# Optimization experiments

Hardware: AMD Instinct MI355X
Metric: run time of the kernel (lower is better)

The kernel has to match this reference:

```python
import jax, jax.numpy as jnp
import numpy as np

C, H, V, N, T = 256, 256, 10000, 8, 256


def _residual_mlp(x, w1, b1, w2, b2, w3, b3):
    # ResidualLayerOld: relu(lin2(relu(lin1(x)))) + x, then final Linear
    h = jax.nn.relu(x @ w1 + b1)
    h = jax.nn.relu(h @ w2 + b2) + x
    return h @ w3 + b3


def setup_inputs() -> dict:
    key = jax.random.key(0)
    ks = jax.random.split(key, 16)
    p = lambda k, shape: jax.random.normal(k, shape, jnp.float32) * 0.02
    return dict(
        text=jax.random.randint(ks[0], (N, T), 0, V),
        mask=jnp.ones((N, T), dtype=bool),
        lengths=jnp.full((N,), T - 1, dtype=jnp.int32),  # full-length sequences
        start_emb=jax.random.normal(ks[1], (C, H), jnp.float32),
        state_emb=jax.random.normal(ks[2], (C, H), jnp.float32),
        preterminal_emb=jax.random.normal(ks[3], (C, H), jnp.float32),
        start_w1=p(ks[4], (H, H)), start_b1=jnp.zeros((H,), jnp.float32),
        start_w2=p(ks[5], (H, H)), start_b2=jnp.zeros((H,), jnp.float32),
        start_w3=p(ks[6], (H, 1)), start_b3=jnp.zeros((1,), jnp.float32),
        trans_w1=p(ks[7], (H, H)), trans_b1=jnp.zeros((H,), jnp.float32),
        trans_w2=p(ks[8], (H, H)), trans_b2=jnp.zeros((H,), jnp.float32),
        trans_w3=p(ks[9], (H, C)), trans_b3=jnp.zeros((C,), jnp.float32),
        term_w1=p(ks[10], (H, H)), term_b1=jnp.zeros((H,), jnp.float32),
        term_w2=p(ks[11], (H, H)), term_b2=jnp.zeros((H,), jnp.float32),
        term_w3=p(ks[12], (H, V)), term_b3=jnp.zeros((V,), jnp.float32),
    )


def _score(text, mask, lengths,
           start_emb, state_emb, preterminal_emb,
           start_w1, start_b1, start_w2, start_b2, start_w3, start_b3,
           trans_w1, trans_b1, trans_w2, trans_b2, trans_w3, trans_b3,
           term_w1, term_b1, term_w2, term_b2, term_w3, term_b3):
    n, t = text.shape
    c = state_emb.shape[0]
    # start / transition / emission distributions (dropout_type == 'none')
    init = jax.nn.log_softmax(
        _residual_mlp(start_emb, start_w1, start_b1, start_w2, start_b2, start_w3, start_b3)[:, 0], -1)  # [C]
    trans = jax.nn.log_softmax(
        _residual_mlp(state_emb, trans_w1, trans_b1, trans_w2, trans_b2, trans_w3, trans_b3), -1)  # [C,C]
    log_em = jax.nn.log_softmax(
        _residual_mlp(preterminal_emb, term_w1, term_b1, term_w2, term_b2, term_w3, term_b3), -1)  # [C,V]
    obs = log_em.T[text]  # [N,T,C], log p(x_t | z=c)
    # torch_struct LinearChain.hmm edge potentials: phi[n,t,c_next,c_prev]
    phi = trans[None, None] + obs[:, 1:, :, None]  # [N,T-1,C,C]
    phi = phi.at[:, 0].add(init[None, None, :] + obs[:, 0][:, None, :])
    phi_t = jnp.swapaxes(phi, 0, 1)  # [T-1,N,C,C]

    def fwd_step(alpha, p):
        new = jax.nn.logsumexp(p + alpha[:, None, :], axis=-1)  # reduce over c_prev
        return new, new

    _, alphas = jax.lax.scan(fwd_step, jnp.zeros((n, c), phi.dtype), phi_t)  # [T-1,N,C]

    def bwd_step(beta, p):
        new = jax.nn.logsumexp(p + beta[:, :, None], axis=1)  # reduce over c_next
        return new, beta

    _, betas = jax.lax.scan(bwd_step, jnp.zeros((n, c), phi.dtype), phi_t, reverse=True)  # [T-1,N,C]

    alpha_prev = jnp.concatenate([jnp.zeros((1, n, c), phi.dtype), alphas[:-1]], 0)
    log_Z = jax.nn.logsumexp(alphas[-1], -1)  # [N]
    # edge posteriors
    log_m = alpha_prev[:, :, None, :] + phi_t + betas[:, :, :, None] - log_Z[None, :, None, None]
    marginals = jnp.swapaxes(jnp.exp(log_m), 0, 1)  # [N,T-1,C,C]

    evidence = jax.nn.logsumexp(alphas[lengths - 1, jnp.arange(n)], -1).sum()
    elbo = jnp.where(mask[:, 1:, None, None],
                     jax.lax.stop_gradient(marginals) * phi,
                     0.0).sum()
    return elbo, evidence


def reference(text, mask, lengths,
              start_emb, state_emb, preterminal_emb,
              start_w1, start_b1, start_w2, start_b2, start_w3, start_b3,
              trans_w1, trans_b1, trans_w2, trans_b2, trans_w3, trans_b3,
              term_w1, term_b1, term_w2, term_b2, term_w3, term_b3):
    elbo, evidence = _score(text, mask, lengths,
                            start_emb, state_emb, preterminal_emb,
                            start_w1, start_b1, start_w2, start_b2, start_w3, start_b3,
                            trans_w1, trans_b1, trans_w2, trans_b2, trans_w3, trans_b3,
                            term_w1, term_b1, term_w2, term_b2, term_w3, term_b3)
    return elbo, evidence
```

## Files before the change

kernel.cpp:

```cpp
#include <hip/hip_runtime.h>
#include <hip/hip_bf16.h>

#define C_ 256
#define H_ 256
#define V_ 10000
#define N_ 8
#define T_ 256
#define TM1_ 255
#define NB_ ((V_ + 31) / 32)
#define VT_ ((V_ + 31) / 32)
#define CH_ 32
#define NCH_ (T_ / CH_)

typedef _Float16 h2_t __attribute__((ext_vector_type(2)));
typedef _Float16 h4_t __attribute__((ext_vector_type(4)));
typedef _Float16 h8_t __attribute__((ext_vector_type(8)));
typedef float f4v __attribute__((ext_vector_type(4)));

__device__ __forceinline__ void bar_lgkm() {
  asm volatile("s_waitcnt lgkmcnt(0)\ns_barrier" ::: "memory");
}

__device__ __forceinline__ float wave_red_max(float v) {
#define DPP_MAX(ctrl) { int iv_ = __float_as_int(v); \
  int r_ = __builtin_amdgcn_update_dpp(iv_, iv_, ctrl, 0xF, 0xF, false); \
  v = fmaxf(v, __int_as_float(r_)); }
  DPP_MAX(0x111) DPP_MAX(0x112) DPP_MAX(0x114) DPP_MAX(0x118)
  DPP_MAX(0x142) DPP_MAX(0x143)
#undef DPP_MAX
  return __int_as_float(__builtin_amdgcn_readlane(__float_as_int(v), 63));
}
__device__ __forceinline__ float wave_red_sum(float v) {
#define DPP_ADD(ctrl) { \
  int r_ = __builtin_amdgcn_update_dpp(0, __float_as_int(v), ctrl, 0xF, 0xF, true); \
  v += __int_as_float(r_); }
  DPP_ADD(0x111) DPP_ADD(0x112) DPP_ADD(0x114) DPP_ADD(0x118)
  DPP_ADD(0x142) DPP_ADD(0x143)
#undef DPP_ADD
  return __int_as_float(__builtin_amdgcn_readlane(__float_as_int(v), 63));
}

__device__ __forceinline__ float block_allmax(float v, float* red) {
  v = wave_red_max(v);
  if ((threadIdx.x & 63) == 0) red[threadIdx.x >> 6] = v;
  __syncthreads();
  v = fmaxf(fmaxf(red[0], red[1]), fmaxf(red[2], red[3]));
  __syncthreads();
  return v;
}
__device__ __forceinline__ float block_allsum(float v, float* red) {
  v = wave_red_sum(v);
  if ((threadIdx.x & 63) == 0) red[threadIdx.x >> 6] = v;
  __syncthreads();
  v = (red[0] + red[1]) + (red[2] + red[3]);
  __syncthreads();
  return v;
}

__global__ __launch_bounds__(256) void k_w3t(const float* __restrict__ w3,
                                             float* __restrict__ w3T) {
  __shared__ float t_s[32][33];
  const int tx = threadIdx.x & 31;
  const int ty = threadIdx.x >> 5;
  const int v0 = blockIdx.x * 32;
  const int k0 = blockIdx.y * 32;
#pragma unroll
  for (int r = 0; r < 4; ++r) {
    int k = k0 + ty + r * 8;
    int v = v0 + tx;
    if (v < V_) t_s[ty + r * 8][tx] = w3[k * V_ + v];
  }
  __syncthreads();
#pragma unroll
  for (int r = 0; r < 4; ++r) {
    int v = v0 + ty + r * 8;
    if (v < V_) w3T[(size_t)v * H_ + k0 + tx] = t_s[tx][ty + r * 8];
  }
}

__device__ __forceinline__ void mlp4(
    const float* __restrict__ emb,
    const float* __restrict__ w1, const float* __restrict__ b1,
    const float* __restrict__ w2, const float* __restrict__ b2,
    int r0, float (&e_s)[4][C_], float (&h_s)[4][C_], float (&h2_s)[4][C_]) {
  const int tid = threadIdx.x;
#pragma unroll
  for (int rr = 0; rr < 4; ++rr)
    e_s[rr][tid] = emb[(r0 + rr) * H_ + tid];
  __syncthreads();
  float bb = b1[tid];
  float a0 = bb, a1 = bb, a2 = bb, a3 = bb;
  for (int k4 = 0; k4 < H_ / 4; ++k4) {
    float4 e0 = ((const float4*)e_s[0])[k4];
    float4 e1 = ((const float4*)e_s[1])[k4];
    float4 e2 = ((const float4*)e_s[2])[k4];
    float4 e3 = ((const float4*)e_s[3])[k4];
    const float* wp = w1 + (k4 * 4) * H_ + tid;
    float wa = wp[0], wb = wp[H_], wc = wp[2 * H_], wd = wp[3 * H_];
    a0 = fmaf(e0.x, wa, a0); a0 = fmaf(e0.y, wb, a0);
    a0 = fmaf(e0.z, wc, a0); a0 = fmaf(e0.w, wd, a0);
    a1 = fmaf(e1.x, wa, a1); a1 = fmaf(e1.y, wb, a1);
    a1 = fmaf(e1.z, wc, a1); a1 = fmaf(e1.w, wd, a1);
    a2 = fmaf(e2.x, wa, a2); a2 = fmaf(e2.y, wb, a2);
    a2 = fmaf(e2.z, wc, a2); a2 = fmaf(e2.w, wd, a2);
    a3 = fmaf(e3.x, wa, a3); a3 = fmaf(e3.y, wb, a3);
    a3 = fmaf(e3.z, wc, a3); a3 = fmaf(e3.w, wd, a3);
  }
  h_s[0][tid] = fmaxf(a0, 0.f);
  h_s[1][tid] = fmaxf(a1, 0.f);
  h_s[2][tid] = fmaxf(a2, 0.f);
  h_s[3][tid] = fmaxf(a3, 0.f);
  __syncthreads();
  bb = b2[tid];
  a0 = bb; a1 = bb; a2 = bb; a3 = bb;
  for (int k4 = 0; k4 < H_ / 4; ++k4) {
    float4 e0 = ((const float4*)h_s[0])[k4];
    float4 e1 = ((const float4*)h_s[1])[k4];
    float4 e2 = ((const float4*)h_s[2])[k4];
    float4 e3 = ((const float4*)h_s[3])[k4];
    const float* wp = w2 + (k4 * 4) * H_ + tid;
    float wa = wp[0], wb = wp[H_], wc = wp[2 * H_], wd = wp[3 * H_];
    a0 = fmaf(e0.x, wa, a0); a0 = fmaf(e0.y, wb, a0);
    a0 = fmaf(e0.z, wc, a0); a0 = fmaf(e0.w, wd, a0);
    a1 = fmaf(e1.x, wa, a1); a1 = fmaf(e1.y, wb, a1);
    a1 = fmaf(e1.z, wc, a1); a1 = fmaf(e1.w, wd, a1);
    a2 = fmaf(e2.x, wa, a2); a2 = fmaf(e2.y, wb, a2);
    a2 = fmaf(e2.z, wc, a2); a2 = fmaf(e2.w, wd, a2);
    a3 = fmaf(e3.x, wa, a3); a3 = fmaf(e3.y, wb, a3);
    a3 = fmaf(e3.z, wc, a3); a3 = fmaf(e3.w, wd, a3);
  }
  h2_s[0][tid] = fmaxf(a0, 0.f) + e_s[0][tid];
  h2_s[1][tid] = fmaxf(a1, 0.f) + e_s[1][tid];
  h2_s[2][tid] = fmaxf(a2, 0.f) + e_s[2][tid];
  h2_s[3][tid] = fmaxf(a3, 0.f) + e_s[3][tid];
  __syncthreads();
}

__global__ __launch_bounds__(256) void k_start(
    const float* __restrict__ emb, const float* __restrict__ w1,
    const float* __restrict__ b1, const float* __restrict__ w2,
    const float* __restrict__ b2, const float* __restrict__ w3,
    const float* __restrict__ b3, float* __restrict__ slogit) {
  __shared__ __align__(16) float e_s[4][C_], h_s[4][C_], h2_s[4][C_];
  __shared__ float red[4];
  const int r0 = blockIdx.x * 4;
  const int tid = threadIdx.x;
  mlp4(emb, w1, b1, w2, b2, r0, e_s, h_s, h2_s);
  float w3v = w3[tid];
  float s0 = block_allsum(h2_s[0][tid] * w3v, red);
  float s1 = block_allsum(h2_s[1][tid] * w3v, red);
  float s2 = block_allsum(h2_s[2][tid] * w3v, red);
  float s3 = block_allsum(h2_s[3][tid] * w3v, red);
  if (tid == 0) {
    float bb = b3[0];
    slogit[r0 + 0] = s0 + bb;
    slogit[r0 + 1] = s1 + bb;
    slogit[r0 + 2] = s2 + bb;
    slogit[r0 + 3] = s3 + bb;
  }
}

__global__ void k_init(const float* __restrict__ slogit, float* __restrict__ initv) {
  __shared__ float red[4];
  const int tid = threadIdx.x;
  float x = slogit[tid];
  float m = block_allmax(x, red);
  float se = block_allsum(__expf(x - m), red);
  initv[tid] = x - m - __logf(se);
}

__global__ __launch_bounds__(256) void k_trans(
    const float* __restrict__ emb, const float* __restrict__ w1,
    const float* __restrict__ b1, const float* __restrict__ w2,
    const float* __restrict__ b2, const float* __restrict__ w3,
    const float* __restrict__ b3, float* __restrict__ Pf,
    float* __restrict__ PLf, float* __restrict__ PTf,
    _Float16* __restrict__ P_h, _Float16* __restrict__ PT_h) {
  __shared__ __align__(16) float e_s[4][C_], h_s[4][C_], h2_s[4][C_];
  __shared__ float red[4];
  const int r0 = blockIdx.x * 4;
  const int tid = threadIdx.x;
  mlp4(emb, w1, b1, w2, b2, r0, e_s, h_s, h2_s);
  float lb = b3[tid];
  float l0 = lb, l1 = lb, l2 = lb, l3 = lb;
  for (int k4 = 0; k4 < H_ / 4; ++k4) {
    float4 e0 = ((const float4*)h2_s[0])[k4];
    float4 e1 = ((const float4*)h2_s[1])[k4];
    float4 e2 = ((const float4*)h2_s[2])[k4];
    float4 e3 = ((const float4*)h2_s[3])[k4];
    const float* wp = w3 + (k4 * 4) * C_ + tid;
    float wa = wp[0], wb = wp[C_], wc = wp[2 * C_], wd = wp[3 * C_];
    l0 = fmaf(e0.x, wa, l0); l0 = fmaf(e0.y, wb, l0);
    l0 = fmaf(e0.z, wc, l0); l0 = fmaf(e0.w, wd, l0);
    l1 = fmaf(e1.x, wa, l1); l1 = fmaf(e1.y, wb, l1);
    l1 = fmaf(e1.z, wc, l1); l1 = fmaf(e1.w, wd, l1);
    l2 = fmaf(e2.x, wa, l2); l2 = fmaf(e2.y, wb, l2);
    l2 = fmaf(e2.z, wc, l2); l2 = fmaf(e2.w, wd, l2);
    l3 = fmaf(e3.x, wa, l3); l3 = fmaf(e3.y, wb, l3);
    l3 = fmaf(e3.z, wc, l3); l3 = fmaf(e3.w, wd, l3);
  }
  float lg[4] = {l0, l1, l2, l3};
#pragma unroll
  for (int rr = 0; rr < 4; ++rr) {
    float m = block_allmax(lg[rr], red);
    float e = __expf(lg[rr] - m);
    float se = block_allsum(e, red);
    float p = e / se;
    float tv = lg[rr] - m - __logf(se);
    const int r = r0 + rr;
    Pf[r * C_ + tid] = p;
    PLf[r * C_ + tid] = p * tv;
    PTf[tid * C_ + r] = p;
    P_h[r * C_ + tid] = (_Float16)p;
    PT_h[tid * C_ + r] = (_Float16)p;
  }
}

__global__ __launch_bounds__(256) void k_term_mlp(
    const float* __restrict__ emb, const float* __restrict__ w1,
    const float* __restrict__ b1, const float* __restrict__ w2,
    const float* __restrict__ b2, float* __restrict__ H2,
    float* __restrict__ H2T) {
  __shared__ __align__(16) float e_s[4][C_], h_s[4][C_], h2_s[4][C_];
  const int r0 = blockIdx.x * 4;
  const int tid = threadIdx.x;
  mlp4(emb, w1, b1, w2, b2, r0, e_s, h_s, h2_s);
#pragma unroll
  for (int rr = 0; rr < 4; ++rr) {
    const int r = r0 + rr;
    float v = h2_s[rr][tid];
    H2[r * H_ + tid] = v;
    H2T[tid * C_ + r] = v;
  }
}

__global__ __launch_bounds__(256) void k_term_stats(
    const float* __restrict__ H2, const float* __restrict__ w3,
    const float* __restrict__ b3, float* __restrict__ partm,
    float* __restrict__ parts) {
  __shared__ __align__(16) float w3_s[H_][32];
  __shared__ float b3_s[32];
  const int v0 = blockIdx.x * 32;
  const int tid = threadIdx.x;
  const int ncols = min(32, V_ - v0);
  for (int idx = tid; idx < H_ * 32; idx += 256) {
    int k = idx >> 5, c = idx & 31;
    w3_s[k][c] = (c < ncols) ? w3[k * V_ + v0 + c] : 0.f;
  }
  if (tid < 32) b3_s[tid] = (tid < ncols) ? b3[v0 + tid] : 0.f;
  __syncthreads();
  float acc[32];
#pragma unroll
  for (int c = 0; c < 32; ++c) acc[c] = 0.f;
  const float4* hq = (const float4*)(H2 + tid * H_);
  for (int k4 = 0; k4 < H_ / 4; ++k4) {
    float4 h = hq[k4];
    float hk[4];
    *(float4*)hk = h;
#pragma unroll
    for (int kk = 0; kk < 4; ++kk) {
      float hv = hk[kk];
      const int k = k4 * 4 + kk;
      const float4* wq = (const float4*)(&w3_s[k][0]);
#pragma unroll
      for (int c4 = 0; c4 < 8; ++c4) {
        float4 w = wq[c4];
        acc[c4 * 4 + 0] = fmaf(hv, w.x, acc[c4 * 4 + 0]);
        acc[c4 * 4 + 1] = fmaf(hv, w.y, acc[c4 * 4 + 1]);
        acc[c4 * 4 + 2] = fmaf(hv, w.z, acc[c4 * 4 + 2]);
        acc[c4 * 4 + 3] = fmaf(hv, w.w, acc[c4 * 4 + 3]);
      }
    }
  }
  float m = -1e30f;
#pragma unroll
  for (int c = 0; c < 32; ++c) {
    acc[c] += b3_s[c];
    if (c < ncols) m = fmaxf(m, acc[c]);
  }
  float se = 0.f;
#pragma unroll
  for (int c = 0; c < 32; ++c)
    if (c < ncols) se += __expf(acc[c] - m);
  partm[blockIdx.x * C_ + tid] = m;
  parts[blockIdx.x * C_ + tid] = se;
}

__global__ void k_denom(const float* __restrict__ partm,
                        const float* __restrict__ parts,
                        float* __restrict__ denom) {
  const int r = threadIdx.x;
  float m = -1e30f;
#pragma unroll 8
  for (int b = 0; b < NB_; ++b) m = fmaxf(m, partm[b * C_ + r]);
  float s = 0.f;
#pragma unroll 8
  for (int b = 0; b < NB_; ++b)
    s += parts[b * C_ + r] * __expf(partm[b * C_ + r] - m);
  denom[r] = m + __logf(s);
}

__global__ __launch_bounds__(256) void k_obs4(
    const int* __restrict__ text, const float* __restrict__ H2T,
    const float* __restrict__ w3T, const float* __restrict__ b3,
    const float* __restrict__ denom, float* __restrict__ EOBS,
    _Float16* __restrict__ EOBSh, float* __restrict__ Karr) {
  __shared__ __align__(16) float w_s[H_][8];
  __shared__ float redm[4][8];
  const int c = threadIdx.x;
  const int wid = c >> 6;
  const int lane = c & 63;
  const int base = blockIdx.x * 8;
  int tok[8];
#pragma unroll
  for (int i = 0; i < 8; ++i) tok[i] = text[base + i];
  float wtmp[8];
#pragma unroll
  for (int i = 0; i < 8; ++i) wtmp[i] = w3T[(size_t)tok[i] * H_ + c];
  float b3t[8];
#pragma unroll
  for (int i = 0; i < 8; ++i) b3t[i] = b3[tok[i]];
#pragma unroll
  for (int i = 0; i < 8; ++i) w_s[c][i] = wtmp[i];
  __syncthreads();
  float acc[8];
#pragma unroll
  for (int i = 0; i < 8; ++i) acc[i] = 0.f;
  for (int k4 = 0; k4 < H_ / 4; ++k4) {
    float hv[4];
#pragma unroll
    for (int kk = 0; kk < 4; ++kk) hv[kk] = H2T[(k4 * 4 + kk) * C_ + c];
#pragma unroll
    for (int kk = 0; kk < 4; ++kk) {
      const float4* wq = (const float4*)(&w_s[k4 * 4 + kk][0]);
      float4 wa = wq[0], wb = wq[1];
      acc[0] = fmaf(hv[kk], wa.x, acc[0]);
      acc[1] = fmaf(hv[kk], wa.y, acc[1]);
      acc[2] = fmaf(hv[kk], wa.z, acc[2]);
      acc[3] = fmaf(hv[kk], wa.w, acc[3]);
      acc[4] = fmaf(hv[kk], wb.x, acc[4]);
      acc[5] = fmaf(hv[kk], wb.y, acc[5]);
      acc[6] = fmaf(hv[kk], wb.z, acc[6]);
      acc[7] = fmaf(hv[kk], wb.w, acc[7]);
    }
  }
  float dn = denom[c];
  float obsv[8];
#pragma unroll
  for (int i = 0; i < 8; ++i) obsv[i] = acc[i] + b3t[i] - dn;
#pragma unroll
  for (int i = 0; i < 8; ++i) {
    float wm = wave_red_max(obsv[i]);
    if (lane == 0) redm[wid][i] = wm;
  }
  __syncthreads();
#pragma unroll
  for (int i = 0; i < 8; ++i) {
    float Ki = fmaxf(fmaxf(redm[0][i], redm[1][i]),
                     fmaxf(redm[2][i], redm[3][i]));
    float ev = __expf(obsv[i] - Ki);
    EOBS[(base + i) * C_ + c] = ev;
    EOBSh[(size_t)(base + i) * C_ + c] = (_Float16)ev;
    if (c == 0) Karr[base + i] = Ki;
  }
}

__global__ __launch_bounds__(256, 1) void k_scan6(
    const _Float16* __restrict__ P_h, const _Float16* __restrict__ PT_h,
    const float* __restrict__ initv, const float* __restrict__ EOBS,
    const _Float16* __restrict__ EOBSh, const float* __restrict__ Karr,
    float* __restrict__ AL, float* __restrict__ BL, float* __restrict__ CC,
    float* __restrict__ DD, float* __restrict__ LOGZ) {
  __shared__ __align__(16) _Float16 eobuf[2][CH_][C_];
  __shared__ __align__(16) _Float16 ubuf[2][C_];
  __shared__ float Kbuf[T_];
  __shared__ float red[4];
  const int tid = threadIdx.x;
  const int wave = tid >> 6;
  const int lane = tid & 63;
  const int quad = lane >> 4;
  const int nn16 = lane & 15;
  const bool bwd = blockIdx.x >= N_;
  const int n = blockIdx.x & (N_ - 1);
  const _Float16* __restrict__ M = bwd ? PT_h : P_h;
  const _Float16* __restrict__ eb = EOBSh + (size_t)n * T_ * C_;

  h8_t afrag[4][8];
#pragma unroll
  for (int mt = 0; mt < 4; ++mt) {
    const _Float16* rp = M + (size_t)((wave << 6) + (mt << 4) + nn16) * C_ + (quad << 3);
#pragma unroll
    for (int kt = 0; kt < 8; ++kt)
      afrag[mt][kt] = *(const h8_t*)(rp + (kt << 5));
  }
  const int stb = (wave << 6) + (quad << 2);

  Kbuf[tid] = Karr[n * T_ + tid];
  {
    const int c0 = bwd ? (NCH_ - 1) : 0;
    const h8_t* g = (const h8_t*)(eb + (size_t)c0 * CH_ * C_);
    h8_t v0 = g[tid], v1 = g[256 + tid], v2 = g[512 + tid], v3 = g[768 + tid];
    h8_t* d = (h8_t*)&eobuf[c0 & 1][0][0];
    d[tid] = v0; d[256 + tid] = v1; d[512 + tid] = v2; d[768 + tid] = v3;
  }
  h8_t pend0, pend1, pend2, pend3;
  {
    const int c1 = bwd ? (NCH_ - 2) : 1;
    const h8_t* g = (const h8_t*)(eb + (size_t)c1 * CH_ * C_);
    pend0 = g[tid]; pend1 = g[256 + tid]; pend2 = g[512 + tid]; pend3 = g[768 + tid];
  }
  __syncthreads();

  if (!bwd) {
    float K0 = Karr[n * T_];
    f4v x0[4];
    float lmax = -1e30f;
#pragma unroll
    for (int mt = 0; mt < 4; ++mt) {
      const int st0 = stb + (mt << 4);
      f4v iv = *(const f4v*)(initv + st0);
      f4v e0 = *(const f4v*)(EOBS + (size_t)(n * T_) * C_ + st0);
#pragma unroll
      for (int r = 0; r < 4; ++r) {
        x0[mt][r] = iv[r] + __logf(e0[r]) + K0;
        lmax = fmaxf(lmax, x0[mt][r]);
      }
    }
    float wm = wave_red_max(lmax);
    if (lane == 0) red[wave] = wm;
    __syncthreads();
    float m0 = fmaxf(fmaxf(red[0], red[1]), fmaxf(red[2], red[3]));
    __syncthreads();
    float Cacc = m0;
    f4v uval[4];
#pragma unroll
    for (int mt = 0; mt < 4; ++mt) {
      const int st0 = stb + (mt << 4);
#pragma unroll
      for (int r = 0; r < 4; ++r) uval[mt][r] = __expf(x0[mt][r] - m0);
      if (nn16 == 0) {
        h4_t p;
#pragma unroll
        for (int r = 0; r < 4; ++r) p[r] = (_Float16)uval[mt][r];
        *(h4_t*)(&ubuf[0][st0]) = p;
        *(f4v*)(AL + (size_t)(0 * N_ + n) * C_ + st0) = uval[mt];
      }
    }
    if (tid == 0) CC[0 * N_ + n] = Cacc;
    float invm = 1.f, logm = 0.f;
    __syncthreads();

#pragma unroll 1
    for (int t = 0; t < TM1_; ++t) {
      const int e = t + 1;
      const int slot = e & 31;
      const int par = (e >> 5) & 1;
      const int cur = t & 1, nxt = cur ^ 1;
      const bool resc = (t & 3) == 3;
      h8_t bf[8];
#pragma unroll
      for (int kt = 0; kt < 8; ++kt)
        bf[kt] = *(const h8_t*)(&ubuf[cur][(kt << 5) + (quad << 3)]);
      h4_t eoh[4];
#pragma unroll
      for (int mt = 0; mt < 4; ++mt)
        eoh[mt] = *(const h4_t*)(&eobuf[par][slot][stb + (mt << 4)]);
      float KA = Kbuf[e];
      f4v ae[4], ao[4];
#pragma unroll
      for (int mt = 0; mt < 4; ++mt) { ae[mt] = (f4v){0, 0, 0, 0}; ao[mt] = (f4v){0, 0, 0, 0}; }
#pragma unroll
      for (int kt = 0; kt < 8; kt += 2) {
#pragma unroll
        for (int mt = 0; mt < 4; ++mt)
          ae[mt] = __builtin_amdgcn_mfma_f32_16x16x32_f16(afrag[mt][kt], bf[kt], ae[mt], 0, 0, 0);
#pragma unroll
        for (int mt = 0; mt < 4; ++mt)
          ao[mt] = __builtin_amdgcn_mfma_f32_16x16x32_f16(afrag[mt][kt + 1], bf[kt + 1], ao[mt], 0, 0, 0);
      }
#pragma unroll
      for (int mt = 0; mt < 4; ++mt) {
#pragma unroll
        for (int r = 0; r < 4; ++r)
          uval[mt][r] = (ae[mt][r] + ao[mt][r]) * invm * (float)eoh[mt][r];
      }
      Cacc += KA + logm;
      if (nn16 == 0) {
#pragma unroll
        for (int mt = 0; mt < 4; ++mt) {
          const int st0 = stb + (mt << 4);
          h4_t p;
#pragma unroll
          for (int r = 0; r < 4; ++r) p[r] = (_Float16)uval[mt][r];
          *(h4_t*)(&ubuf[nxt][st0]) = p;
        }
      }
      if (resc) {
        float lmx = -1e30f;
#pragma unroll
        for (int mt = 0; mt < 4; ++mt)
#pragma unroll
          for (int r = 0; r < 4; ++r) lmx = fmaxf(lmx, uval[mt][r]);
        float wmm = wave_red_max(lmx);
        if (lane == 0) red[wave] = wmm;
      }
      if (slot == 31 && e != 255) {
        const int ci = e >> 5;
        h8_t* d = (h8_t*)&eobuf[(ci + 1) & 1][0][0];
        d[tid] = pend0; d[256 + tid] = pend1; d[512 + tid] = pend2; d[768 + tid] = pend3;
        if (ci + 2 < NCH_) {
          const h8_t* g = (const h8_t*)(eb + (size_t)(ci + 2) * CH_ * C_);
          pend0 = g[tid]; pend1 = g[256 + tid]; pend2 = g[512 + tid]; pend3 = g[768 + tid];
        }
      }
      bar_lgkm();
      if (nn16 == 0) {
#pragma unroll
        for (int mt = 0; mt < 4; ++mt)
          *(f4v*)(AL + (size_t)((t + 1) * N_ + n) * C_ + stb + (mt << 4)) = uval[mt];
      }
      if (tid == 0) CC[(t + 1) * N_ + n] = Cacc;
      if (resc) {
        float m = fmaxf(fmaxf(red[0], red[1]), fmaxf(red[2], red[3]));
        m = fmaxf(m, 1e-30f);
        invm = 1.f / m;
        logm = __logf(m);
      } else { invm = 1.f; logm = 0.f; }
    }
    float s = 0.f;
#pragma unroll
    for (int mt = 0; mt < 4; ++mt)
      s += (uval[mt][0] + uval[mt][1]) + (uval[mt][2] + uval[mt][3]);
    s = wave_red_sum(s);
    if (lane == 0) red[wave] = s;
    __syncthreads();
    float S = ((red[0] + red[1]) + (red[2] + red[3])) * (1.f / 16.f);
    if (tid == 0) LOGZ[n] = __logf(S) + Cacc;
  } else {
    float Dacc = 0.f;
    f4v vval[4];
#pragma unroll
    for (int mt = 0; mt < 4; ++mt) {
      const int st0 = stb + (mt << 4);
      vval[mt] = *(const f4v*)(EOBS + ((size_t)n * T_ + TM1_) * C_ + st0);
      if (nn16 == 0) {
        h4_t p;
#pragma unroll
        for (int r = 0; r < 4; ++r) p[r] = (_Float16)vval[mt][r];
        *(h4_t*)(&ubuf[0][st0]) = p;
        f4v one = (f4v){1.f, 1.f, 1.f, 1.f};
        *(f4v*)(BL + (size_t)((TM1_ - 1) * N_ + n) * C_ + st0) = one;
      }
    }
    if (tid == 0) DD[(TM1_ - 1) * N_ + n] = 0.f;
    __syncthreads();

#pragma unroll 1
    for (int it = 0, t = TM1_ - 2; t >= 0; --t, ++it) {
      const int e = t + 1;
      const int slot = e & 31;
      const int par = (e >> 5) & 1;
      const int cur = it & 1, nxt = cur ^ 1;
      float invm = 1.f, logm = 0.f;
      if ((it & 3) == 3) {
        float m = fmaxf(fmaxf(red[0], red[1]), fmaxf(red[2], red[3]));
        m = fmaxf(m, 1e-30f);
        invm = 1.f / m;
        logm = __logf(m);
      }
      h8_t bf[8];
#pragma unroll
      for (int kt = 0; kt < 8; ++kt)
        bf[kt] = *(const h8_t*)(&ubuf[cur][(kt << 5) + (quad << 3)]);
      h4_t eoh[4];
#pragma unroll
      for (int mt = 0; mt < 4; ++mt)
        eoh[mt] = *(const h4_t*)(&eobuf[par][slot][stb + (mt << 4)]);
      float KA = Kbuf[e + 1];
      f4v ae[4], ao[4];
#pragma unroll
      for (int mt = 0; mt < 4; ++mt) { ae[mt] = (f4v){0, 0, 0, 0}; ao[mt] = (f4v){0, 0, 0, 0}; }
#pragma unroll
      for (int kt = 0; kt < 8; kt += 2) {
#pragma unroll
        for (int mt = 0; mt < 4; ++mt)
          ae[mt] = __builtin_amdgcn_mfma_f32_16x16x32_f16(afrag[mt][kt], bf[kt], ae[mt], 0, 0, 0);
#pragma unroll
        for (int mt = 0; mt < 4; ++mt)
          ao[mt] = __builtin_amdgcn_mfma_f32_16x16x32_f16(afrag[mt][kt + 1], bf[kt + 1], ao[mt], 0, 0, 0);
      }
      Dacc += KA + logm;
      f4v blv[4];
#pragma unroll
      for (int mt = 0; mt < 4; ++mt) {
#pragma unroll
        for (int r = 0; r < 4; ++r) {
          float b = (ae[mt][r] + ao[mt][r]) * invm;
          blv[mt][r] = b;
          vval[mt][r] = b * (float)eoh[mt][r];
        }
      }
      if (((it + 1) & 3) == 3) {
        float lmx = -1e30f;
#pragma unroll
        for (int mt = 0; mt < 4; ++mt)
#pragma unroll
          for (int r = 0; r < 4; ++r) lmx = fmaxf(lmx, vval[mt][r]);
        float wmm = wave_red_max(lmx);
        if (lane == 0) red[wave] = wmm;
      }
      if (nn16 == 0) {
#pragma unroll
        for (int mt = 0; mt < 4; ++mt) {
          const int st0 = stb + (mt << 4);
          h4_t p;
#pragma unroll
          for (int r = 0; r < 4; ++r) p[r] = (_Float16)vval[mt][r];
          *(h4_t*)(&ubuf[nxt][st0]) = p;
        }
      }
      if (slot == 0 && e >= 32) {
        const int ci = e >> 5;
        h8_t* d = (h8_t*)&eobuf[(ci - 1) & 1][0][0];
        d[tid] = pend0; d[256 + tid] = pend1; d[512 + tid] = pend2; d[768 + tid] = pend3;
        if (ci - 2 >= 0) {
          const h8_t* g = (const h8_t*)(eb + (size_t)(ci - 2) * CH_ * C_);
          pend0 = g[tid]; pend1 = g[256 + tid]; pend2 = g[512 + tid]; pend3 = g[768 + tid];
        }
      }
      bar_lgkm();
      if (nn16 == 0) {
#pragma unroll
        for (int mt = 0; mt < 4; ++mt)
          *(f4v*)(BL + (size_t)(t * N_ + n) * C_ + stb + (mt << 4)) = blv[mt];
      }
      if (tid == 0) DD[t * N_ + n] = Dacc;
    }
  }
}

#define NH_ 4
__global__ __launch_bounds__(256) void k_elbo(
    const float* __restrict__ Pf, const float* __restrict__ PLf,
    const float* __restrict__ PTf, const float* __restrict__ AL,
    const float* __restrict__ BL, const float* __restrict__ CC,
    const float* __restrict__ DD, const float* __restrict__ EOBS,
    const float* __restrict__ Karr, const float* __restrict__ LOGZ,
    float* __restrict__ out) {
  __shared__ __align__(16) float A_s[NH_][C_];
  __shared__ __align__(16) float B_s[NH_][C_];
  __shared__ float red[4];
  const int t = blockIdx.x;
  const int nb = blockIdx.y * NH_;
  const int c = threadIdx.x;
  if (t == 0 && blockIdx.y == 0 && c == 0) {
    float s = 0.f;
#pragma unroll
    for (int nn = 0; nn < N_; ++nn) s += LOGZ[nn];
    out[1] = s;
  }
  float sc[NH_], Kv[NH_], cc[NH_];
#pragma unroll
  for (int nn = 0; nn < NH_; ++nn) {
    const int n = nb + nn;
    A_s[nn][c] = AL[(t * N_ + n) * C_ + c];
    Kv[nn] = Karr[n * T_ + t + 1];
    cc[nn] = CC[t * N_ + n];
    sc[nn] = __expf(cc[nn] + DD[t * N_ + n] + Kv[nn] - LOGZ[n]);
  }
  __syncthreads();
  float accPA[NH_], accPL[NH_];
#pragma unroll
  for (int nn = 0; nn < NH_; ++nn) { accPA[nn] = 0.f; accPL[nn] = 0.f; }
  const float4* pr = (const float4*)(Pf + c * C_);
  const float4* plr = (const float4*)(PLf + c * C_);
  for (int j = 0; j < C_ / 4; ++j) {
    float4 p = pr[j];
    float4 pl = plr[j];
#pragma unroll
    for (int nn = 0; nn < NH_; ++nn) {
      float4 a = ((const float4*)A_s[nn])[j];
      accPA[nn] += p.x * a.x + p.y * a.y + p.z * a.z + p.w * a.w;
      accPL[nn] += pl.x * a.x + pl.y * a.y + pl.z * a.z + pl.w * a.w;
    }
  }
  float contrib = 0.f;
  float Bv[NH_];
#pragma unroll
  for (int nn = 0; nn < NH_; ++nn) {
    const int n = nb + nn;
    float eo = EOBS[(n * T_ + t + 1) * C_ + c];
    float ob = __logf(eo) + Kv[nn];
    float B = eo * BL[(t * N_ + n) * C_ + c] * sc[nn];
    Bv[nn] = B;
    contrib += B * fmaf(ob, accPA[nn], accPL[nn]);
  }
  if (t == 0) {
#pragma unroll
    for (int nn = 0; nn < NH_; ++nn) B_s[nn][c] = Bv[nn];
    __syncthreads();
    const float4* ptq = (const float4*)(PTf + c * C_);
    float accPT[NH_];
#pragma unroll
    for (int nn = 0; nn < NH_; ++nn) accPT[nn] = 0.f;
    for (int j = 0; j < C_ / 4; ++j) {
      float4 p = ptq[j];
#pragma unroll
      for (int nn = 0; nn < NH_; ++nn) {
        float4 b = ((const float4*)B_s[nn])[j];
        accPT[nn] += p.x * b.x + p.y * b.y + p.z * b.z + p.w * b.w;
      }
    }
#pragma unroll
    for (int nn = 0; nn < NH_; ++nn) {
      float a0v = A_s[nn][c];
      if (a0v > 0.f)
        contrib += a0v * (__logf(a0v) + cc[nn]) * accPT[nn];
    }
  }
  contrib = wave_red_sum(contrib);
  if ((c & 63) == 0) red[c >> 6] = contrib;
  __syncthreads();
  if (c == 0) atomicAdd(out, (red[0] + red[1]) + (red[2] + red[3]));
}

extern "C" void kernel_launch(void* const* d_in, const int* in_sizes, int n_in,
                              void* d_out, int out_size, void* d_ws, size_t ws_size,
                              hipStream_t stream) {
  (void)in_sizes; (void)n_in; (void)out_size; (void)ws_size;
  const int* text = (const int*)d_in[0];
  const float* start_emb = (const float*)d_in[3];
  const float* state_emb = (const float*)d_in[4];
  const float* pre_emb   = (const float*)d_in[5];
  const float* sw1 = (const float*)d_in[6];  const float* sb1 = (const float*)d_in[7];
  const float* sw2 = (const float*)d_in[8];  const float* sb2 = (const float*)d_in[9];
  const float* sw3 = (const float*)d_in[10]; const float* sb3 = (const float*)d_in[11];
  const float* tw1 = (const float*)d_in[12]; const float* tb1 = (const float*)d_in[13];
  const float* tw2 = (const float*)d_in[14]; const float* tb2 = (const float*)d_in[15];
  const float* tw3 = (const float*)d_in[16]; const float* tb3 = (const float*)d_in[17];
  const float* ew1 = (const float*)d_in[18]; const float* eb1 = (const float*)d_in[19];
  const float* ew2 = (const float*)d_in[20]; const float* eb2 = (const float*)d_in[21];
  const float* ew3 = (const float*)d_in[22]; const float* eb3 = (const float*)d_in[23];
  float* out = (float*)d_out;

  char* p = (char*)d_ws;
  auto alloc = [&](size_t bytes) -> char* {
    char* r = p;
    p += (bytes + 255) & ~(size_t)255;
    return r;
  };
  float* slogit = (float*)alloc(C_ * 4);
  float* initv  = (float*)alloc(C_ * 4);
  float* denom  = (float*)alloc(C_ * 4);
  float* LOGZ   = (float*)alloc(N_ * 4);
  float* Pf     = (float*)alloc(C_ * C_ * 4);
  float* PLf    = (float*)alloc(C_ * C_ * 4);
  float* PTf    = (float*)alloc(C_ * C_ * 4);
  _Float16* P_h  = (_Float16*)alloc(C_ * C_ * 2);
  _Float16* PT_h = (_Float16*)alloc(C_ * C_ * 2);
  float* H2    = (float*)alloc(C_ * H_ * 4);
  float* H2T   = (float*)alloc(C_ * H_ * 4);
  float* partm = (float*)alloc(NB_ * C_ * 4);
  float* parts = (float*)alloc(NB_ * C_ * 4);
  float* w3T   = (float*)alloc((size_t)V_ * H_ * 4);
  float* EOBS  = (float*)alloc((size_t)N_ * T_ * C_ * 4);
  _Float16* EOBSh = (_Float16*)alloc((size_t)N_ * T_ * C_ * 2);
  float* Karr  = (float*)alloc((size_t)N_ * T_ * 4);
  float* AL    = (float*)alloc((size_t)T_ * N_ * C_ * 4);
  float* BL    = (float*)alloc((size_t)TM1_ * N_ * C_ * 4);
  float* CC    = (float*)alloc((size_t)T_ * N_ * 4);
  float* DD    = (float*)alloc((size_t)TM1_ * N_ * 4);

  hipMemsetAsync(d_out, 0, 2 * sizeof(float), stream);

  k_w3t<<<dim3(VT_, H_ / 32), dim3(256), 0, stream>>>(ew3, w3T);
  k_start<<<dim3(C_ / 4), dim3(256), 0, stream>>>(start_emb, sw1, sb1, sw2, sb2, sw3, sb3, slogit);
  k_init<<<dim3(1), dim3(256), 0, stream>>>(slogit, initv);
  k_trans<<<dim3(C_ / 4), dim3(256), 0, stream>>>(state_emb, tw1, tb1, tw2, tb2, tw3, tb3,
                                                  Pf, PLf, PTf, P_h, PT_h);
  k_term_mlp<<<dim3(C_ / 4), dim3(256), 0, stream>>>(pre_emb, ew1, eb1, ew2, eb2, H2, H2T);
  k_term_stats<<<dim3(NB_), dim3(256), 0, stream>>>(H2, ew3, eb3, partm, parts);
  k_denom<<<dim3(1), dim3(256), 0, stream>>>(partm, parts, denom);
  k_obs4<<<dim3(N_ * T_ / 8), dim3(256), 0, stream>>>(text, H2T, w3T, eb3, denom,
                                                      EOBS, EOBSh, Karr);
  k_scan6<<<dim3(2 * N_), dim3(256), 0, stream>>>(P_h, PT_h, initv, EOBS, EOBSh, Karr,
                                                  AL, BL, CC, DD, LOGZ);
  k_elbo<<<dim3(TM1_, 2), dim3(256), 0, stream>>>(Pf, PLf, PTf, AL, BL, CC, DD,
                                                  EOBS, Karr, LOGZ, out);
}
```

Before: 566.5 us.

## Merge forward and backward scans into one 512-thread block per sequence

After: 651.9 us. 1.15x slower.

```diff
diff --git a/kernel.cpp b/kernel.cpp
--- a/kernel.cpp
+++ b/kernel.cpp
@@ -9,7 +9,7 @@
 #define TM1_ 255
 #define NB_ ((V_ + 31) / 32)
 #define VT_ ((V_ + 31) / 32)
-#define CH_ 32
+#define CH_ 16
 #define NCH_ (T_ / CH_)
 
 typedef _Float16 h2_t __attribute__((ext_vector_type(2)));
@@ -300,11 +300,11 @@
   denom[r] = m + __logf(s);
 }
 
-__global__ __launch_bounds__(256) void k_obs4(
+__global__ __launch_bounds__(256) void k_obs3(
     const int* __restrict__ text, const float* __restrict__ H2T,
     const float* __restrict__ w3T, const float* __restrict__ b3,
     const float* __restrict__ denom, float* __restrict__ EOBS,
-    _Float16* __restrict__ EOBSh, float* __restrict__ Karr) {
+    float* __restrict__ Karr) {
   __shared__ __align__(16) float w_s[H_][8];
   __shared__ float redm[4][8];
   const int c = threadIdx.x;
@@ -358,32 +358,33 @@
   for (int i = 0; i < 8; ++i) {
     float Ki = fmaxf(fmaxf(redm[0][i], redm[1][i]),
                      fmaxf(redm[2][i], redm[3][i]));
-    float ev = __expf(obsv[i] - Ki);
-    EOBS[(base + i) * C_ + c] = ev;
-    EOBSh[(size_t)(base + i) * C_ + c] = (_Float16)ev;
+    EOBS[(base + i) * C_ + c] = __expf(obsv[i] - Ki);
     if (c == 0) Karr[base + i] = Ki;
   }
 }
 
-__global__ __launch_bounds__(256, 1) void k_scan6(
+__global__ __launch_bounds__(512, 1) void k_scan7(
     const _Float16* __restrict__ P_h, const _Float16* __restrict__ PT_h,
     const float* __restrict__ initv, const float* __restrict__ EOBS,
-    const _Float16* __restrict__ EOBSh, const float* __restrict__ Karr,
-    float* __restrict__ AL, float* __restrict__ BL, float* __restrict__ CC,
-    float* __restrict__ DD, float* __restrict__ LOGZ) {
-  __shared__ __align__(16) _Float16 eobuf[2][CH_][C_];
-  __shared__ __align__(16) _Float16 ubuf[2][C_];
+    const float* __restrict__ Karr, float* __restrict__ AL,
+    float* __restrict__ BL, float* __restrict__ CC, float* __restrict__ DD,
+    float* __restrict__ LOGZ) {
+  __shared__ __align__(16) float eobufF[2][CH_][C_];
+  __shared__ __align__(16) float eobufB[2][CH_][C_];
+  __shared__ __align__(16) _Float16 ubufF[2][C_];
+  __shared__ __align__(16) _Float16 ubufB[2][C_];
   __shared__ float Kbuf[T_];
-  __shared__ float red[4];
+  __shared__ float redF[4], redB[4];
   const int tid = threadIdx.x;
-  const int wave = tid >> 6;
+  const int grp = tid >> 8;
+  const int gtid = tid & 255;
+  const int wave = gtid >> 6;
   const int lane = tid & 63;
   const int quad = lane >> 4;
   const int nn16 = lane & 15;
-  const bool bwd = blockIdx.x >= N_;
-  const int n = blockIdx.x & (N_ - 1);
-  const _Float16* __restrict__ M = bwd ? PT_h : P_h;
-  const _Float16* __restrict__ eb = EOBSh + (size_t)n * T_ * C_;
+  const int n = blockIdx.x;
+  const _Float16* __restrict__ M = grp ? PT_h : P_h;
+  const float* __restrict__ ebase = EOBS + (size_t)n * T_ * C_;
 
   h8_t afrag[4][8];
 #pragma unroll
@@ -395,31 +396,36 @@
   }
   const int stb = (wave << 6) + (quad << 2);
 
-  Kbuf[tid] = Karr[n * T_ + tid];
+  if (tid < 256) Kbuf[tid] = Karr[n * T_ + tid];
   {
-    const int c0 = bwd ? (NCH_ - 1) : 0;
-    const h8_t* g = (const h8_t*)(eb + (size_t)c0 * CH_ * C_);
-    h8_t v0 = g[tid], v1 = g[256 + tid], v2 = g[512 + tid], v3 = g[768 + tid];
-    h8_t* d = (h8_t*)&eobuf[c0 & 1][0][0];
-    d[tid] = v0; d[256 + tid] = v1; d[512 + tid] = v2; d[768 + tid] = v3;
-  }
-  h8_t pend0, pend1, pend2, pend3;
+    const int c0 = grp ? (NCH_ - 1) : 0;
+    const f4v* g = (const f4v*)(ebase + (size_t)c0 * CH_ * C_);
+    f4v v0 = g[gtid], v1 = g[256 + gtid], v2 = g[512 + gtid], v3 = g[768 + gtid];
+    f4v* d = (f4v*)(grp ? &eobufB[c0 & 1][0][0] : &eobufF[c0 & 1][0][0]);
+    d[gtid] = v0; d[256 + gtid] = v1; d[512 + gtid] = v2; d[768 + gtid] = v3;
+  }
+  f4v pd0, pd1, pd2, pd3;
   {
-    const int c1 = bwd ? (NCH_ - 2) : 1;
-    const h8_t* g = (const h8_t*)(eb + (size_t)c1 * CH_ * C_);
-    pend0 = g[tid]; pend1 = g[256 + tid]; pend2 = g[512 + tid]; pend3 = g[768 + tid];
-  }
-  __syncthreads();
-
-  if (!bwd) {
-    float K0 = Karr[n * T_];
-    f4v x0[4];
+    const int c1 = grp ? (NCH_ - 2) : 1;
+    const f4v* g = (const f4v*)(ebase + (size_t)c1 * CH_ * C_);
+    pd0 = g[gtid]; pd1 = g[256 + gtid]; pd2 = g[512 + gtid]; pd3 = g[768 + gtid];
+  }
+  __syncthreads();
+
+  float invm = 1.f, logm = 0.f;
+  float Cacc = 0.f, Dacc = 0.f;
+  f4v uval[4];
+  f4v blv[4];
+  f4v x0[4];
+
+  if (grp == 0) {
+    float K0 = Kbuf[0];
     float lmax = -1e30f;
 #pragma unroll
     for (int mt = 0; mt < 4; ++mt) {
       const int st0 = stb + (mt << 4);
       f4v iv = *(const f4v*)(initv + st0);
-      f4v e0 = *(const f4v*)(EOBS + (size_t)(n * T_) * C_ + st0);
+      f4v e0 = *(const f4v*)(&eobufF[0][0][st0]);
 #pragma unroll
       for (int r = 0; r < 4; ++r) {
         x0[mt][r] = iv[r] + __logf(e0[r]) + K0;
@@ -427,12 +433,28 @@
       }
     }
     float wm = wave_red_max(lmax);
-    if (lane == 0) red[wave] = wm;
-    __syncthreads();
-    float m0 = fmaxf(fmaxf(red[0], red[1]), fmaxf(red[2], red[3]));
-    __syncthreads();
-    float Cacc = m0;
-    f4v uval[4];
+    if (lane == 0) redF[wave] = wm;
+  } else {
+#pragma unroll
+    for (int mt = 0; mt < 4; ++mt) {
+      const int st0 = stb + (mt << 4);
+      uval[mt] = *(const f4v*)(&eobufB[(NCH_ - 1) & 1][CH_ - 1][st0]);
+      if (nn16 == 0) {
+        h4_t p;
+#pragma unroll
+        for (int r = 0; r < 4; ++r) p[r] = (_Float16)uval[mt][r];
+        *(h4_t*)(&ubufB[0][st0]) = p;
+        f4v one = (f4v){1.f, 1.f, 1.f, 1.f};
+        *(f4v*)(BL + (size_t)((TM1_ - 1) * N_ + n) * C_ + st0) = one;
+      }
+    }
+    if (tid == 256) DD[(TM1_ - 1) * N_ + n] = 0.f;
+  }
+  __syncthreads();
+
+  if (grp == 0) {
+    float m0 = fmaxf(fmaxf(redF[0], redF[1]), fmaxf(redF[2], redF[3]));
+    Cacc = m0;
 #pragma unroll
     for (int mt = 0; mt < 4; ++mt) {
       const int st0 = stb + (mt << 4);
@@ -442,29 +464,30 @@
         h4_t p;
 #pragma unroll
         for (int r = 0; r < 4; ++r) p[r] = (_Float16)uval[mt][r];
-        *(h4_t*)(&ubuf[0][st0]) = p;
+        *(h4_t*)(&ubufF[0][st0]) = p;
         *(f4v*)(AL + (size_t)(0 * N_ + n) * C_ + st0) = uval[mt];
       }
     }
     if (tid == 0) CC[0 * N_ + n] = Cacc;
-    float invm = 1.f, logm = 0.f;
-    __syncthreads();
+  }
+  __syncthreads();
 
 #pragma unroll 1
-    for (int t = 0; t < TM1_; ++t) {
-      const int e = t + 1;
-      const int slot = e & 31;
-      const int par = (e >> 5) & 1;
-      const int cur = t & 1, nxt = cur ^ 1;
-      const bool resc = (t & 3) == 3;
+  for (int it = 0; it < TM1_; ++it) {
+    const int cur = it & 1, nxt = cur ^ 1;
+    const bool resc = (it & 3) == 3;
+    if (grp == 0) {
+      const int e = it + 1;
+      const int slot = e & (CH_ - 1);
+      const int par = (e >> 4) & 1;
       h8_t bf[8];
 #pragma unroll
       for (int kt = 0; kt < 8; ++kt)
-        bf[kt] = *(const h8_t*)(&ubuf[cur][(kt << 5) + (quad << 3)]);
-      h4_t eoh[4];
+        bf[kt] = *(const h8_t*)(&ubufF[cur][(kt << 5) + (quad << 3)]);
+      f4v eo[4];
 #pragma unroll
       for (int mt = 0; mt < 4; ++mt)
-        eoh[mt] = *(const h4_t*)(&eobuf[par][slot][stb + (mt << 4)]);
+        eo[mt] = *(const f4v*)(&eobufF[par][slot][stb + (mt << 4)]);
       float KA = Kbuf[e];
       f4v ae[4], ao[4];
 #pragma unroll
@@ -479,11 +502,10 @@
           ao[mt] = __builtin_amdgcn_mfma_f32_16x16x32_f16(afrag[mt][kt + 1], bf[kt + 1], ao[mt], 0, 0, 0);
       }
 #pragma unroll
-      for (int mt = 0; mt < 4; ++mt) {
+      for (int mt = 0; mt < 4; ++mt)
 #pragma unroll
         for (int r = 0; r < 4; ++r)
-          uval[mt][r] = (ae[mt][r] + ao[mt][r]) * invm * (float)eoh[mt][r];
-      }
+          uval[mt][r] = (ae[mt][r] + ao[mt][r]) * invm * eo[mt][r];
       Cacc += KA + logm;
       if (nn16 == 0) {
 #pragma unroll
@@ -492,7 +514,7 @@
           h4_t p;
 #pragma unroll
           for (int r = 0; r < 4; ++r) p[r] = (_Float16)uval[mt][r];
-          *(h4_t*)(&ubuf[nxt][st0]) = p;
+          *(h4_t*)(&ubufF[nxt][st0]) = p;
         }
       }
       if (resc) {
@@ -502,140 +524,125 @@
 #pragma unroll
           for (int r = 0; r < 4; ++r) lmx = fmaxf(lmx, uval[mt][r]);
         float wmm = wave_red_max(lmx);
-        if (lane == 0) red[wave] = wmm;
-      }
-      if (slot == 31 && e != 255) {
-        const int ci = e >> 5;
-        h8_t* d = (h8_t*)&eobuf[(ci + 1) & 1][0][0];
-        d[tid] = pend0; d[256 + tid] = pend1; d[512 + tid] = pend2; d[768 + tid] = pend3;
+        if (lane == 0) redF[wave] = wmm;
+      }
+      if (slot == CH_ - 1 && e != 255) {
+        const int ci = e >> 4;
+        f4v* d = (f4v*)&eobufF[(ci + 1) & 1][0][0];
+        d[gtid] = pd0; d[256 + gtid] = pd1; d[512 + gtid] = pd2; d[768 + gtid] = pd3;
         if (ci + 2 < NCH_) {
-          const h8_t* g = (const h8_t*)(eb + (size_t)(ci + 2) * CH_ * C_);
-          pend0 = g[tid]; pend1 = g[256 + tid]; pend2 = g[512 + tid]; pend3 = g[768 + tid];
+          const f4v* g = (const f4v*)(ebase + (size_t)(ci + 2) * CH_ * C_);
+          pd0 = g[gtid]; pd1 = g[256 + gtid]; pd2 = g[512 + gtid]; pd3 = g[768 + gtid];
         }
       }
-      bar_lgkm();
+    } else if (it < TM1_ - 1) {
+      const int e = 254 - it;
+      const int slot = e & (CH_ - 1);
+      const int par = (e >> 4) & 1;
+      float binvm = 1.f, blogm = 0.f;
+      if ((it & 3) == 3) {
+        float m = fmaxf(fmaxf(redB[0], redB[1]), fmaxf(redB[2], redB[3]));
+        m = fmaxf(m, 1e-30f);
+        binvm = 1.f / m;
+        blogm = __logf(m);
+      }
+      h8_t bf[8];
+#pragma unroll
+      for (int kt = 0; kt < 8; ++kt)
+        bf[kt] = *(const h8_t*)(&ubufB[cur][(kt << 5) + (quad << 3)]);
+      f4v eo[4];
+#pragma unroll
+      for (int mt = 0; mt < 4; ++mt)
+        eo[mt] = *(const f4v*)(&eobufB[par][slot][stb + (mt << 4)]);
+      float KA = Kbuf[e + 1];
+      f4v ae[4], ao[4];
+#pragma unroll
+      for (int mt = 0; mt < 4; ++mt) { ae[mt] = (f4v){0, 0, 0, 0}; ao[mt] = (f4v){0, 0, 0, 0}; }
+#pragma unroll
+      for (int kt = 0; kt < 8; kt += 2) {
+#pragma unroll
+        for (int mt = 0; mt < 4; ++mt)
+          ae[mt] = __builtin_amdgcn_mfma_f32_16x16x32_f16(afrag[mt][kt], bf[kt], ae[mt], 0, 0, 0);
+#pragma unroll
+        for (int mt = 0; mt < 4; ++mt)
+          ao[mt] = __builtin_amdgcn_mfma_f32_16x16x32_f16(afrag[mt][kt + 1], bf[kt + 1], ao[mt], 0, 0, 0);
+      }
+      Dacc += KA + blogm;
+#pragma unroll
+      for (int mt = 0; mt < 4; ++mt) {
+#pragma unroll
+        for (int r = 0; r < 4; ++r) {
+          float b = (ae[mt][r] + ao[mt][r]) * binvm;
+          blv[mt][r] = b;
+          uval[mt][r] = b * eo[mt][r];
+        }
+      }
+      if (((it + 1) & 3) == 3) {
+        float lmx = -1e30f;
+#pragma unroll
+        for (int mt = 0; mt < 4; ++mt)
+#pragma unroll
+          for (int r = 0; r < 4; ++r) lmx = fmaxf(lmx, uval[mt][r]);
+        float wmm = wave_red_max(lmx);
+        if (lane == 0) redB[wave] = wmm;
+      }
       if (nn16 == 0) {
 #pragma unroll
+        for (int mt = 0; mt < 4; ++mt) {
+          const int st0 = stb + (mt << 4);
+          h4_t p;
+#pragma unroll
+          for (int r = 0; r < 4; ++r) p[r] = (_Float16)uval[mt][r];
+          *(h4_t*)(&ubufB[nxt][st0]) = p;
+        }
+      }
+      if (slot == 0 && e >= CH_) {
+        const int ci = e >> 4;
+        f4v* d = (f4v*)&eobufB[(ci - 1) & 1][0][0];
+        d[gtid] = pd0; d[256 + gtid] = pd1; d[512 + gtid] = pd2; d[768 + gtid] = pd3;
+        if (ci - 2 >= 0) {
+          const f4v* g = (const f4v*)(ebase + (size_t)(ci - 2) * CH_ * C_);
+          pd0 = g[gtid]; pd1 = g[256 + gtid]; pd2 = g[512 + gtid]; pd3 = g[768 + gtid];
+        }
+      }
+    }
+    bar_lgkm();
+    if (grp == 0) {
+      if (nn16 == 0) {
+#pragma unroll
         for (int mt = 0; mt < 4; ++mt)
-          *(f4v*)(AL + (size_t)((t + 1) * N_ + n) * C_ + stb + (mt << 4)) = uval[mt];
-      }
-      if (tid == 0) CC[(t + 1) * N_ + n] = Cacc;
+          *(f4v*)(AL + (size_t)((it + 1) * N_ + n) * C_ + stb + (mt << 4)) = uval[mt];
+      }
+      if (tid == 0) CC[(it + 1) * N_ + n] = Cacc;
       if (resc) {
-        float m = fmaxf(fmaxf(red[0], red[1]), fmaxf(red[2], red[3]));
+        float m = fmaxf(fmaxf(redF[0], redF[1]), fmaxf(redF[2], redF[3]));
         m = fmaxf(m, 1e-30f);
         invm = 1.f / m;
         logm = __logf(m);
       } else { invm = 1.f; logm = 0.f; }
-    }
+    } else if (it < TM1_ - 1) {
+      const int t = 253 - it;
+      if (nn16 == 0) {
+#pragma unroll
+        for (int mt = 0; mt < 4; ++mt)
+          *(f4v*)(BL + (size_t)(t * N_ + n) * C_ + stb + (mt << 4)) = blv[mt];
+      }
+      if (tid == 256) DD[t * N_ + n] = Dacc;
+    }
+  }
+
+  if (grp == 0) {
     float s = 0.f;
 #pragma unroll
     for (int mt = 0; mt < 4; ++mt)
       s += (uval[mt][0] + uval[mt][1]) + (uval[mt][2] + uval[mt][3]);
     s = wave_red_sum(s);
-    if (lane == 0) red[wave] = s;
-    __syncthreads();
-    float S = ((red[0] + red[1]) + (red[2] + red[3])) * (1.f / 16.f);
-    if (tid == 0) LOGZ[n] = __logf(S) + Cacc;
-  } else {
-    float Dacc = 0.f;
-    f4v vval[4];
-#pragma unroll
-    for (int mt = 0; mt < 4; ++mt) {
-      const int st0 = stb + (mt << 4);
-      vval[mt] = *(const f4v*)(EOBS + ((size_t)n * T_ + TM1_) * C_ + st0);
-      if (nn16 == 0) {
-        h4_t p;
-#pragma unroll
-        for (int r = 0; r < 4; ++r) p[r] = (_Float16)vval[mt][r];
-        *(h4_t*)(&ubuf[0][st0]) = p;
-        f4v one = (f4v){1.f, 1.f, 1.f, 1.f};
-        *(f4v*)(BL + (size_t)((TM1_ - 1) * N_ + n) * C_ + st0) = one;
-      }
-    }
-    if (tid == 0) DD[(TM1_ - 1) * N_ + n] = 0.f;
-    __syncthreads();
-
-#pragma unroll 1
-    for (int it = 0, t = TM1_ - 2; t >= 0; --t, ++it) {
-      const int e = t + 1;
-      const int slot = e & 31;
-      const int par = (e >> 5) & 1;
-      const int cur = it & 1, nxt = cur ^ 1;
-      float invm = 1.f, logm = 0.f;
-      if ((it & 3) == 3) {
-        float m = fmaxf(fmaxf(red[0], red[1]), fmaxf(red[2], red[3]));
-        m = fmaxf(m, 1e-30f);
-        invm = 1.f / m;
-        logm = __logf(m);
-      }
-      h8_t bf[8];
-#pragma unroll
-      for (int kt = 0; kt < 8; ++kt)
-        bf[kt] = *(const h8_t*)(&ubuf[cur][(kt << 5) + (quad << 3)]);
-      h4_t eoh[4];
-#pragma unroll
-      for (int mt = 0; mt < 4; ++mt)
-        eoh[mt] = *(const h4_t*)(&eobuf[par][slot][stb + (mt << 4)]);
-      float KA = Kbuf[e + 1];
-      f4v ae[4], ao[4];
-#pragma unroll
-      for (int mt = 0; mt < 4; ++mt) { ae[mt] = (f4v){0, 0, 0, 0}; ao[mt] = (f4v){0, 0, 0, 0}; }
-#pragma unroll
-      for (int kt = 0; kt < 8; kt += 2) {
-#pragma unroll
-        for (int mt = 0; mt < 4; ++mt)
-          ae[mt] = __builtin_amdgcn_mfma_f32_16x16x32_f16(afrag[mt][kt], bf[kt], ae[mt], 0, 0, 0);
-#pragma unroll
-        for (int mt = 0; mt < 4; ++mt)
-          ao[mt] = __builtin_amdgcn_mfma_f32_16x16x32_f16(afrag[mt][kt + 1], bf[kt + 1], ao[mt], 0, 0, 0);
-      }
-      Dacc += KA + logm;
-      f4v blv[4];
-#pragma unroll
-      for (int mt = 0; mt < 4; ++mt) {
-#pragma unroll
-        for (int r = 0; r < 4; ++r) {
-          float b = (ae[mt][r] + ao[mt][r]) * invm;
-          blv[mt][r] = b;
-          vval[mt][r] = b * (float)eoh[mt][r];
-        }
-      }
-      if (((it + 1) & 3) == 3) {
-        float lmx = -1e30f;
-#pragma unroll
-        for (int mt = 0; mt < 4; ++mt)
-#pragma unroll
-          for (int r = 0; r < 4; ++r) lmx = fmaxf(lmx, vval[mt][r]);
-        float wmm = wave_red_max(lmx);
-        if (lane == 0) red[wave] = wmm;
-      }
-      if (nn16 == 0) {
-#pragma unroll
-        for (int mt = 0; mt < 4; ++mt) {
-          const int st0 = stb + (mt << 4);
-          h4_t p;
-#pragma unroll
-          for (int r = 0; r < 4; ++r) p[r] = (_Float16)vval[mt][r];
-          *(h4_t*)(&ubuf[nxt][st0]) = p;
-        }
-      }
-      if (slot == 0 && e >= 32) {
-        const int ci = e >> 5;
-        h8_t* d = (h8_t*)&eobuf[(ci - 1) & 1][0][0];
-        d[tid] = pend0; d[256 + tid] = pend1; d[512 + tid] = pend2; d[768 + tid] = pend3;
-        if (ci - 2 >= 0) {
-          const h8_t* g = (const h8_t*)(eb + (size_t)(ci - 2) * CH_ * C_);
-          pend0 = g[tid]; pend1 = g[256 + tid]; pend2 = g[512 + tid]; pend3 = g[768 + tid];
-        }
-      }
-      bar_lgkm();
-      if (nn16 == 0) {
-#pragma unroll
-        for (int mt = 0; mt < 4; ++mt)
-          *(f4v*)(BL + (size_t)(t * N_ + n) * C_ + stb + (mt << 4)) = blv[mt];
-      }
-      if (tid == 0) DD[t * N_ + n] = Dacc;
-    }
+    if (lane == 0) redF[wave] = s;
+  }
+  __syncthreads();
+  if (grp == 0 && tid == 0) {
+    float S = ((redF[0] + redF[1]) + (redF[2] + redF[3])) * (1.f / 16.f);
+    LOGZ[n] = __logf(S) + Cacc;
   }
 }
 
@@ -764,7 +771,6 @@
   float* parts = (float*)alloc(NB_ * C_ * 4);
   float* w3T   = (float*)alloc((size_t)V_ * H_ * 4);
   float* EOBS  = (float*)alloc((size_t)N_ * T_ * C_ * 4);
-  _Float16* EOBSh = (_Float16*)alloc((size_t)N_ * T_ * C_ * 2);
   float* Karr  = (float*)alloc((size_t)N_ * T_ * 4);
   float* AL    = (float*)alloc((size_t)T_ * N_ * C_ * 4);
   float* BL    = (float*)alloc((size_t)TM1_ * N_ * C_ * 4);
@@ -781,10 +787,9 @@
   k_term_mlp<<<dim3(C_ / 4), dim3(256), 0, stream>>>(pre_emb, ew1, eb1, ew2, eb2, H2, H2T);
   k_term_stats<<<dim3(NB_), dim3(256), 0, stream>>>(H2, ew3, eb3, partm, parts);
   k_denom<<<dim3(1), dim3(256), 0, stream>>>(partm, parts, denom);
-  k_obs4<<<dim3(N_ * T_ / 8), dim3(256), 0, stream>>>(text, H2T, w3T, eb3, denom,
-                                                      EOBS, EOBSh, Karr);
-  k_scan6<<<dim3(2 * N_), dim3(256), 0, stream>>>(P_h, PT_h, initv, EOBS, EOBSh, Karr,
-                                                  AL, BL, CC, DD, LOGZ);
+  k_obs3<<<dim3(N_ * T_ / 8), dim3(256), 0, stream>>>(text, H2T, w3T, eb3, denom, EOBS, Karr);
+  k_scan7<<<dim3(N_), dim3(512), 0, stream>>>(P_h, PT_h, initv, EOBS, Karr,
+                                              AL, BL, CC, DD, LOGZ);
   k_elbo<<<dim3(TM1_, 2), dim3(256), 0, stream>>>(Pf, PLf, PTf, AL, BL, CC, DD,
                                                   EOBS, Karr, LOGZ, out);
 }
```
